# Performance work log

Measured on AMD Instinct MI355X. Metric: run time of the kernel, lower is better.

Reference implementation:

```python
import jax, jax.numpy as jnp
import numpy as np

TEMPERATURE = 2.718281828459045  # math.e
N_EXPERTS = 64
N_ACTIVE = 44  # int(64 * 0.7)
EPS = 1e-08


def setup_inputs() -> dict:
    key = jax.random.key(0)
    k1, k2 = jax.random.split(key)
    B, S, D = 4, 4096, 2048
    x = jax.random.normal(k1, (B, S, D), dtype=jnp.float32)
    # xavier_uniform for Linear(D, E): bound = sqrt(6 / (D + E))
    bound = float(np.sqrt(6.0 / (D + N_EXPERTS)))
    gate_w = jax.random.uniform(k2, (N_EXPERTS, D), dtype=jnp.float32,
                                minval=-bound, maxval=bound)
    return {"x": x, "gate_w": gate_w}


def reference(x, gate_w):
    B, S, D = x.shape
    E = gate_w.shape[0]
    # gate + temperature
    scores = jnp.einsum("bsd,ed->bse", x, gate_w) / TEMPERATURE
    probs = jax.nn.softmax(scores, axis=-1)  # (B, S, E)
    topk_vals, topk_idx = jax.lax.top_k(probs, N_ACTIVE)  # (B, S, K)
    # scatter 1.0 into mask at top-k indices (flatten token dims)
    flat_idx = topk_idx.reshape(-1, N_ACTIVE)  # (N, K)
    rows = jnp.arange(flat_idx.shape[0])[:, None]  # (N, 1)
    mask = jnp.zeros((flat_idx.shape[0], E), dtype=probs.dtype)
    mask = mask.at[rows, flat_idx].set(1.0).reshape(B, S, E)
    weights = probs * mask
    weights = weights / (jnp.sum(weights, axis=-1, keepdims=True) + EPS)
    return weights
```

## Files before the change

### kernel.cpp

```cpp
#include <hip/hip_runtime.h>
#include <hip/hip_bf16.h>


#define NTOK   16384
#define DIM    2048
#define NEXP   64
#define NACT   44
#define BM     64
#define BK     64
#define NSTEPS (DIM / BK)

__device__ __forceinline__ void gload16(const float* g, float* l) {
  __builtin_amdgcn_global_load_lds(
      (const __attribute__((address_space(1))) void*)g,
      (__attribute__((address_space(3))) void*)l, 16, 0, 0);
}

__global__ __launch_bounds__(256) void boltzmann_router_kernel(
    const float* __restrict__ x, const float* __restrict__ gw,
    float* __restrict__ out) {
  __shared__ float xs[2][BM * BK];
  __shared__ float wsm[2][NEXP * BK];

  const int t    = threadIdx.x;
  const int wv   = t >> 6;
  const int ln   = t & 63;
  const int tok0 = blockIdx.x * BM;

  const int tm = t & 15;
  const int te = t >> 4;
  const int m0 = tm * 4, e0 = te * 4;

  double acc[4][4] = {};

  const int lrow = ln >> 4;
  const int lc16 = ln & 15;

  #pragma unroll
  for (int i = 0; i < 4; ++i) {
    const int chunk = wv * 4 + i;
    const int r = chunk * 4 + lrow;
    const int c = (lc16 ^ chunk) * 4;
    gload16(x  + (size_t)(tok0 + r) * DIM + c, &xs[0][chunk * 256]);
    gload16(gw + (size_t)r          * DIM + c, &wsm[0][chunk * 256]);
  }
  __syncthreads();

  for (int step = 0; step < NSTEPS; ++step) {
    const int cur = step & 1;
    if (step + 1 < NSTEPS) {
      const int k0 = (step + 1) * BK;
      const int nb = cur ^ 1;
      #pragma unroll
      for (int i = 0; i < 4; ++i) {
        const int chunk = wv * 4 + i;
        const int r = chunk * 4 + lrow;
        const int c = (lc16 ^ chunk) * 4;
        gload16(x  + (size_t)(tok0 + r) * DIM + k0 + c, &xs[nb][chunk * 256]);
        gload16(gw + (size_t)r          * DIM + k0 + c, &wsm[nb][chunk * 256]);
      }
    }
    const float4* xa = reinterpret_cast<const float4*>(&xs[cur][0]);
    const float4* wa = reinterpret_cast<const float4*>(&wsm[cur][0]);
    #pragma unroll 4
    for (int kk = 0; kk < 16; ++kk) {
      float4 a[4], b[4];
      #pragma unroll
      for (int m = 0; m < 4; ++m) a[m] = xa[(m0 + m) * 16 + (kk ^ tm)];
      #pragma unroll
      for (int e = 0; e < 4; ++e) b[e] = wa[(e0 + e) * 16 + (kk ^ te)];
      double bd[4][4];
      #pragma unroll
      for (int e = 0; e < 4; ++e) {
        bd[e][0] = (double)b[e].x; bd[e][1] = (double)b[e].y;
        bd[e][2] = (double)b[e].z; bd[e][3] = (double)b[e].w;
      }
      #pragma unroll
      for (int m = 0; m < 4; ++m) {
        const double ax = (double)a[m].x, ay = (double)a[m].y;
        const double az = (double)a[m].z, aw = (double)a[m].w;
        #pragma unroll
        for (int e = 0; e < 4; ++e) {
          acc[m][e] = fma(ax, bd[e][0], acc[m][e]);
          acc[m][e] = fma(ay, bd[e][1], acc[m][e]);
          acc[m][e] = fma(az, bd[e][2], acc[m][e]);
          acc[m][e] = fma(aw, bd[e][3], acc[m][e]);
        }
      }
    }
    __syncthreads();
  }

  double* sc = reinterpret_cast<double*>(&xs[0][0]);
  const double INVT = 0.36787944117144233;
  #pragma unroll
  for (int m = 0; m < 4; ++m)
    #pragma unroll
    for (int e = 0; e < 4; ++e)
      sc[(m0 + m) * 64 + (e0 + e)] = acc[m][e] * INVT;
  __syncthreads();

  for (int it = 0; it < 16; ++it) {
    const int m = wv * 16 + it;
    const double s64 = sc[m * 64 + ln];

    double v = s64;
    #pragma unroll
    for (int k = 2; k <= 64; k <<= 1) {
      #pragma unroll
      for (int j = k >> 1; j > 0; j >>= 1) {
        const double o  = __shfl_xor(v, j, 64);
        const bool up  = ((ln & k) == 0);
        const bool low = ((ln & j) == 0);
        v = (low == up) ? fmin(v, o) : fmax(v, o);
      }
    }
    const double thr = __shfl(v, 64 - NACT, 64);
    const bool sel = (s64 >= thr);

    const float s = (float)s64;
    float mx = s;
    #pragma unroll
    for (int j = 32; j > 0; j >>= 1) mx = fmaxf(mx, __shfl_xor(mx, j, 64));
    const float ex = __expf(s - mx);
    float sum = ex;
    #pragma unroll
    for (int j = 32; j > 0; j >>= 1) sum += __shfl_xor(sum, j, 64);
    const float p = ex / sum;

    float ps = sel ? p : 0.0f;
    #pragma unroll
    for (int j = 32; j > 0; j >>= 1) ps += __shfl_xor(ps, j, 64);

    out[(size_t)(tok0 + m) * NEXP + ln] = sel ? (p / (ps + 1e-8f)) : 0.0f;
  }
}

extern "C" void kernel_launch(void* const* d_in, const int* in_sizes, int n_in,
                              void* d_out, int out_size, void* d_ws, size_t ws_size,
                              hipStream_t stream) {
  const float* x  = (const float*)d_in[0];
  const float* gw = (const float*)d_in[1];
  float* out = (float*)d_out;
  boltzmann_router_kernel<<<dim3(NTOK / BM), dim3(256), 0, stream>>>(x, gw, out);
}
```

Baseline: 326.9 us.

## Compute gate scores in fp32 with fp64 recompute only for near-tie thresholds

Replaces the fp64 FMA GEMM with an fp32 accumulation in which each lane owns one expert and reads a wave's 8 token rows directly through scalar/constant loads. Only the gate weights are staged in LDS. When the gap between the 20th and 21st sorted score is below a small epsilon, the token's scores are recomputed in fp64 from global memory to keep top-k selection exact. The aim is to remove the slow fp64 arithmetic that dominated the kernel. The risks are lower parallelism per block, scalar-load bandwidth limits, and a divergent slow fallback path.

Result: slower. 454.0 us (+38.9%).

```diff
diff --git a/kernel.cpp b/kernel.cpp
--- a/kernel.cpp
+++ b/kernel.cpp
@@ -1,14 +1,20 @@
 #include <hip/hip_runtime.h>
-#include <hip/hip_bf16.h>
 
 
 #define NTOK   16384
 #define DIM    2048
 #define NEXP   64
 #define NACT   44
-#define BM     64
-#define BK     64
-#define NSTEPS (DIM / BK)
+#define TPW    8
+#define NWAVE  4
+#define BM     (TPW * NWAVE)
+#define BK     128
+#define NSTEP  (DIM / BK)
+#define NCHUNK (BK / 8)
+#define GAP_EPS 2e-4f
+
+typedef float f4 __attribute__((ext_vector_type(4)));
+typedef const __attribute__((address_space(4))) f4* cf4p;
 
 __device__ __forceinline__ void gload16(const float* g, float* l) {
   __builtin_amdgcn_global_load_lds(
@@ -16,123 +22,140 @@
       (__attribute__((address_space(3))) void*)l, 16, 0, 0);
 }
 
+__device__ __forceinline__ float wave_max(float v) {
+  #pragma unroll
+  for (int j = 32; j > 0; j >>= 1) v = fmaxf(v, __shfl_xor(v, j, 64));
+  return v;
+}
+__device__ __forceinline__ float wave_sum(float v) {
+  #pragma unroll
+  for (int j = 32; j > 0; j >>= 1) v += __shfl_xor(v, j, 64);
+  return v;
+}
+
 __global__ __launch_bounds__(256) void boltzmann_router_kernel(
     const float* __restrict__ x, const float* __restrict__ gw,
     float* __restrict__ out) {
-  __shared__ float xs[2][BM * BK];
-  __shared__ float wsm[2][NEXP * BK];
+  __shared__ float wlds[2][NEXP * BK];
 
-  const int t    = threadIdx.x;
-  const int wv   = t >> 6;
-  const int ln   = t & 63;
-  const int tok0 = blockIdx.x * BM;
+  const int t  = threadIdx.x;
+  const int ln = t & 63;
+  const int wv = __builtin_amdgcn_readfirstlane(t >> 6);
+  const int tokw = blockIdx.x * BM + wv * TPW;
 
-  const int tm = t & 15;
-  const int te = t >> 4;
-  const int m0 = tm * 4, e0 = te * 4;
+  const int lrow = ln >> 5;
+  const int slot = ln & 31;
 
-  double acc[4][4] = {};
+  #define STAGE(b, K0)                                                    \
+    {                                                                     \
+      _Pragma("unroll")                                                   \
+      for (int i = 0; i < 8; ++i) {                                       \
+        const int chunk = wv * 8 + i;                   \
+        const int r = 2 * chunk + lrow;                 \
+        const int sg = slot ^ (r & 7);                 \
+        gload16(gw + r * DIM + (K0) + sg * 4, &wlds[b][chunk * 256]);     \
+      }                                                                   \
+    }
 
-  const int lrow = ln >> 4;
-  const int lc16 = ln & 15;
+  STAGE(0, 0);
 
-  #pragma unroll
-  for (int i = 0; i < 4; ++i) {
-    const int chunk = wv * 4 + i;
-    const int r = chunk * 4 + lrow;
-    const int c = (lc16 ^ chunk) * 4;
-    gload16(x  + (size_t)(tok0 + r) * DIM + c, &xs[0][chunk * 256]);
-    gload16(gw + (size_t)r          * DIM + c, &wsm[0][chunk * 256]);
-  }
+  float acc[TPW][2] = {};
+  const unsigned long long xbase =
+      (unsigned long long)(const void*)(x + (size_t)tokw * DIM);
+
   __syncthreads();
 
-  for (int step = 0; step < NSTEPS; ++step) {
+  for (int step = 0; step < NSTEP; ++step) {
     const int cur = step & 1;
-    if (step + 1 < NSTEPS) {
-      const int k0 = (step + 1) * BK;
-      const int nb = cur ^ 1;
+    if (step + 1 < NSTEP) STAGE(cur ^ 1, (step + 1) * BK);
+
+    const f4* wp = reinterpret_cast<const f4*>(&wlds[cur][0]);
+    cf4p xp = reinterpret_cast<cf4p>(xbase + (unsigned long long)step * BK * 4);
+
+    #pragma unroll 2
+    for (int c = 0; c < NCHUNK; ++c) {
+      const int s0 = 2 * c, s1 = 2 * c + 1;
+      const f4 w0 = wp[ln * 32 + (s0 ^ (ln & 7))];
+      const f4 w1 = wp[ln * 32 + (s1 ^ (ln & 7))];
       #pragma unroll
-      for (int i = 0; i < 4; ++i) {
-        const int chunk = wv * 4 + i;
-        const int r = chunk * 4 + lrow;
-        const int c = (lc16 ^ chunk) * 4;
-        gload16(x  + (size_t)(tok0 + r) * DIM + k0 + c, &xs[nb][chunk * 256]);
-        gload16(gw + (size_t)r          * DIM + k0 + c, &wsm[nb][chunk * 256]);
-      }
-    }
-    const float4* xa = reinterpret_cast<const float4*>(&xs[cur][0]);
-    const float4* wa = reinterpret_cast<const float4*>(&wsm[cur][0]);
-    #pragma unroll 4
-    for (int kk = 0; kk < 16; ++kk) {
-      float4 a[4], b[4];
-      #pragma unroll
-      for (int m = 0; m < 4; ++m) a[m] = xa[(m0 + m) * 16 + (kk ^ tm)];
-      #pragma unroll
-      for (int e = 0; e < 4; ++e) b[e] = wa[(e0 + e) * 16 + (kk ^ te)];
-      double bd[4][4];
-      #pragma unroll
-      for (int e = 0; e < 4; ++e) {
-        bd[e][0] = (double)b[e].x; bd[e][1] = (double)b[e].y;
-        bd[e][2] = (double)b[e].z; bd[e][3] = (double)b[e].w;
-      }
-      #pragma unroll
-      for (int m = 0; m < 4; ++m) {
-        const double ax = (double)a[m].x, ay = (double)a[m].y;
-        const double az = (double)a[m].z, aw = (double)a[m].w;
-        #pragma unroll
-        for (int e = 0; e < 4; ++e) {
-          acc[m][e] = fma(ax, bd[e][0], acc[m][e]);
-          acc[m][e] = fma(ay, bd[e][1], acc[m][e]);
-          acc[m][e] = fma(az, bd[e][2], acc[m][e]);
-          acc[m][e] = fma(aw, bd[e][3], acc[m][e]);
-        }
+      for (int tt = 0; tt < TPW; ++tt) {
+        const f4 a0 = xp[tt * (DIM / 4) + s0];
+        const f4 a1 = xp[tt * (DIM / 4) + s1];
+        float u = acc[tt][0], v = acc[tt][1];
+        u = fmaf(a0.x, w0.x, u); u = fmaf(a0.y, w0.y, u);
+        u = fmaf(a0.z, w0.z, u); u = fmaf(a0.w, w0.w, u);
+        v = fmaf(a1.x, w1.x, v); v = fmaf(a1.y, w1.y, v);
+        v = fmaf(a1.z, w1.z, v); v = fmaf(a1.w, w1.w, v);
+        acc[tt][0] = u; acc[tt][1] = v;
       }
     }
     __syncthreads();
   }
 
-  double* sc = reinterpret_cast<double*>(&xs[0][0]);
-  const double INVT = 0.36787944117144233;
-  #pragma unroll
-  for (int m = 0; m < 4; ++m)
-    #pragma unroll
-    for (int e = 0; e < 4; ++e)
-      sc[(m0 + m) * 64 + (e0 + e)] = acc[m][e] * INVT;
-  __syncthreads();
+  const float INVT = 0.36787944117144233f;
+  #pragma unroll 1
+  for (int tt = 0; tt < TPW; ++tt) {
+    const int tok = tokw + tt;
+    const float s = (acc[tt][0] + acc[tt][1]) * INVT;
 
-  for (int it = 0; it < 16; ++it) {
-    const int m = wv * 16 + it;
-    const double s64 = sc[m * 64 + ln];
-
-    double v = s64;
+    float v = s;
     #pragma unroll
     for (int k = 2; k <= 64; k <<= 1) {
       #pragma unroll
       for (int j = k >> 1; j > 0; j >>= 1) {
-        const double o  = __shfl_xor(v, j, 64);
-        const bool up  = ((ln & k) == 0);
-        const bool low = ((ln & j) == 0);
-        v = (low == up) ? fmin(v, o) : fmax(v, o);
+        const float o = __shfl_xor(v, j, 64);
+        const bool up = ((ln & k) == 0);
+        const bool lo = ((ln & j) == 0);
+        v = (lo == up) ? fminf(v, o) : fmaxf(v, o);
       }
     }
-    const double thr = __shfl(v, 64 - NACT, 64);
-    const bool sel = (s64 >= thr);
+    const float v20 = __shfl(v, 64 - NACT, 64);
+    const float v19 = __shfl(v, 64 - NACT - 1, 64);
 
-    const float s = (float)s64;
-    float mx = s;
-    #pragma unroll
-    for (int j = 32; j > 0; j >>= 1) mx = fmaxf(mx, __shfl_xor(mx, j, 64));
-    const float ex = __expf(s - mx);
-    float sum = ex;
-    #pragma unroll
-    for (int j = 32; j > 0; j >>= 1) sum += __shfl_xor(sum, j, 64);
+    bool sel;
+    float sv = s;
+    if (v20 - v19 < GAP_EPS) {
+      const f4* xr = reinterpret_cast<const f4*>(x + (size_t)tok * DIM);
+      const f4* wr = reinterpret_cast<const f4*>(gw + (size_t)ln * DIM);
+      double p0=0,p1=0,p2=0,p3=0,p4=0,p5=0,p6=0,p7=0;
+      for (int k = 0; k < DIM / 8; ++k) {
+        const f4 xa = xr[2*k], xb = xr[2*k+1];
+        const f4 wa = wr[2*k], wb = wr[2*k+1];
+        p0 = fma((double)xa.x, (double)wa.x, p0);
+        p1 = fma((double)xa.y, (double)wa.y, p1);
+        p2 = fma((double)xa.z, (double)wa.z, p2);
+        p3 = fma((double)xa.w, (double)wa.w, p3);
+        p4 = fma((double)xb.x, (double)wb.x, p4);
+        p5 = fma((double)xb.y, (double)wb.y, p5);
+        p6 = fma((double)xb.z, (double)wb.z, p6);
+        p7 = fma((double)xb.w, (double)wb.w, p7);
+      }
+      const double s64 =
+          (((p0+p1)+(p2+p3)) + ((p4+p5)+(p6+p7))) * 0.36787944117144233;
+      double dv = s64;
+      #pragma unroll
+      for (int k = 2; k <= 64; k <<= 1) {
+        #pragma unroll
+        for (int j = k >> 1; j > 0; j >>= 1) {
+          const double o = __shfl_xor(dv, j, 64);
+          const bool up = ((ln & k) == 0);
+          const bool lo = ((ln & j) == 0);
+          dv = (lo == up) ? fmin(dv, o) : fmax(dv, o);
+        }
+      }
+      const double thr64 = __shfl(dv, 64 - NACT, 64);
+      sel = (s64 >= thr64);
+      sv = (float)s64;
+    } else {
+      sel = (s >= v20);
+    }
+
+    const float mx = wave_max(sv);
+    const float ex = __expf(sv - mx);
+    const float sum = wave_sum(ex);
     const float p = ex / sum;
-
-    float ps = sel ? p : 0.0f;
-    #pragma unroll
-    for (int j = 32; j > 0; j >>= 1) ps += __shfl_xor(ps, j, 64);
-
-    out[(size_t)(tok0 + m) * NEXP + ln] = sel ? (p / (ps + 1e-8f)) : 0.0f;
+    const float ps = wave_sum(sel ? p : 0.0f);
+    out[(size_t)tok * NEXP + ln] = sel ? (p / (ps + 1e-8f)) : 0.0f;
   }
 }
 
```
